# Kernel tuning notes

Measured on AMD Instinct MI355X. Metric: run time of the kernel, lower is better.

## Reference

```python
import jax, jax.numpy as jnp
import numpy as np

N_HEADS = 16

def _rotate_half(t):
    # t: [B, H, T, hs]; split last dim in half, return cat(-x2, x1)
    hs = t.shape[-1]
    x1, x2 = t[..., : hs // 2], t[..., hs // 2 :]
    return jnp.concatenate((-x2, x1), axis=-1)

def _rope_pos(T, hs, dtype):
    inv_freq = 1.0 / (10000.0 ** (jnp.arange(0, hs, 2, dtype=jnp.float32) / hs))
    freqs = jnp.arange(T, dtype=jnp.float32)[:, None] * inv_freq[None, :]  # [T, hs/2]
    pos = jnp.concatenate((freqs, freqs), axis=-1)  # [T, hs]
    return pos

def setup_inputs() -> dict:
    key = jax.random.key(0)
    ks = jax.random.split(key, 5)
    d = 2048
    x = jax.random.normal(ks[0], (2, 2048, d), dtype=jnp.float32)
    W_attn = jax.random.normal(ks[1], (d, 3 * d), dtype=jnp.float32) * (1.0 / np.sqrt(d))
    b_attn = jax.random.normal(ks[2], (3 * d,), dtype=jnp.float32) * 0.02
    W_proj = jax.random.normal(ks[3], (d, d), dtype=jnp.float32) * (1.0 / np.sqrt(d))
    b_proj = jax.random.normal(ks[4], (d,), dtype=jnp.float32) * 0.02
    return {"x": x, "W_attn": W_attn, "b_attn": b_attn, "W_proj": W_proj, "b_proj": b_proj}

def reference(x, W_attn, b_attn, W_proj, b_proj):
    B, T, C = x.shape
    nh = N_HEADS
    hs = C // nh
    qkv = x @ W_attn + b_attn  # [B, T, 3C]
    q, k, v = jnp.split(qkv, 3, axis=-1)
    # [B, T, C] -> [B, nh, T, hs]
    def to_heads(t):
        return t.reshape(B, T, nh, hs).transpose(0, 2, 1, 3)
    q, k, v = to_heads(q), to_heads(k), to_heads(v)
    # RoPE
    pos = _rope_pos(T, hs, x.dtype)  # [T, hs]
    cos, sin = jnp.cos(pos).astype(x.dtype), jnp.sin(pos).astype(x.dtype)
    q = q * cos + _rotate_half(q) * sin
    k = k * cos + _rotate_half(k) * sin
    # causal SDPA
    scale = 1.0 / np.sqrt(hs)
    scores = jnp.einsum('bhqd,bhkd->bhqk', q, k) * scale  # [B, nh, T, T]
    causal = jnp.tril(jnp.ones((T, T), dtype=bool))
    scores = jnp.where(causal, scores, jnp.finfo(scores.dtype).min)
    att = jax.nn.softmax(scores, axis=-1)
    out = jnp.einsum('bhqk,bhkd->bhqd', att, v)  # [B, nh, T, hs]
    y = out.transpose(0, 2, 1, 3).reshape(B, T, C)
    return y @ W_proj + b_proj
```

## Files before the change

kernel.cpp:

```cpp
#include <hip/hip_runtime.h>
#include <stdint.h>

typedef unsigned short u16;
typedef __attribute__((ext_vector_type(8))) short short8;
typedef __attribute__((ext_vector_type(4))) float f32x4;
typedef __attribute__((ext_vector_type(4))) unsigned short u16x4;

#define DEV __device__ __forceinline__

DEV u16 f2bf(float f) {
  union { float f; unsigned u; } v; v.f = f;
  unsigned r = v.u + 0x7fffu + ((v.u >> 16) & 1u);
  return (u16)(r >> 16);
}
DEV float bf2f(u16 b) {
  union { unsigned u; float f; } v; v.u = ((unsigned)b) << 16;
  return v.f;
}
DEV void gload_lds16(const void* g, void* l) {
  __builtin_amdgcn_global_load_lds((const __attribute__((address_space(1))) void*)g,
                                   (__attribute__((address_space(3))) void*)l,
                                   16, 0, 0);
}
DEV void block_barrier() {
  asm volatile("" ::: "memory");
  __builtin_amdgcn_s_barrier();
  asm volatile("" ::: "memory");
}

__global__ void k_conv(const float* __restrict__ in, u16* __restrict__ out, int n4) {
  int i = blockIdx.x * blockDim.x + threadIdx.x;
  if (i >= n4) return;
  const f32x4 v = *(const f32x4*)(in + (size_t)i * 4);
  u16x4 o;
  o[0] = f2bf(v[0]); o[1] = f2bf(v[1]); o[2] = f2bf(v[2]); o[3] = f2bf(v[3]);
  *(u16x4*)(out + (size_t)i * 4) = o;
}

__global__ void k_tconv(const float* __restrict__ in, u16* __restrict__ out, int R, int C) {
  __shared__ float tile[32][33];
  int c0 = blockIdx.x * 32, r0 = blockIdx.y * 32;
  int tx = threadIdx.x, ty = threadIdx.y;
#pragma unroll
  for (int j = 0; j < 32; j += 8)
    tile[ty + j][tx] = in[(size_t)(r0 + ty + j) * C + (c0 + tx)];
  __syncthreads();
#pragma unroll
  for (int j = 0; j < 32; j += 8)
    out[(size_t)(c0 + ty + j) * R + (r0 + tx)] = f2bf(tile[tx][ty + j]);
}

__global__ void k_rtab(float* __restrict__ ct, float* __restrict__ st) {
  int id = blockIdx.x * 256 + threadIdx.x;
  int t = id >> 6, dd = id & 63;
  float inv = exp2f((float)dd * -0.20762050593045077f);
  float s, c;
  sincosf((float)t * inv, &s, &c);
  ct[id] = c; st[id] = s;
}

__global__ __launch_bounds__(512, 2) void k_gemmqkv(const u16* __restrict__ A,
                                                    const u16* __restrict__ Bt,
                                                    const float* __restrict__ bias,
                                                    u16* __restrict__ qh,
                                                    u16* __restrict__ kh,
                                                    u16* __restrict__ vt,
                                                    const float* __restrict__ rtab) {
  const int Kld = 2048, nt = 32;
  __shared__ __align__(16) short smem[4][256 * 64];
  const int tid = threadIdx.x;
  const int wid = tid >> 6, lane = tid & 63;
  const int gx = gridDim.x;
  const int nwg = gx * gridDim.y;
  const int orig = blockIdx.y * gx + blockIdx.x;
  const int lg = (orig & 7) * (nwg >> 3) + (orig >> 3);
  const int bm = (lg % gx) * 256, bn = (lg / gx) * 256;
  const int wr = wid >> 2, wc = wid & 3;
  const int r = lane & 15, kq = lane >> 4, r7 = lane & 7;

  int aoff[4], boff[4], lbase[4];
#pragma unroll
  for (int j = 0; j < 4; ++j) {
    int c = j * 512 + wid * 64 + lane;
    int row = c >> 3, ch = c & 7;
    aoff[j] = (bm + row) * Kld + (ch ^ (row & 7)) * 8;
    boff[j] = (bn + row) * Kld + (ch ^ (row & 7)) * 8;
    lbase[j] = (j * 512 + wid * 64) * 16;
  }

#define STG_A(k0, buf, j) gload_lds16(A + aoff[j] + (k0), (char*)&smem[(buf)][0] + lbase[j])
#define STG_B(k0, buf, j) gload_lds16(Bt + boff[j] + (k0), (char*)&smem[2 + (buf)][0] + lbase[j])
#define RD_A(AF, MH, KK)                                                        \
  _Pragma("unroll")                                                             \
  for (int m2 = 0; m2 < 4; ++m2)                                                \
    AF[m2] = *(const short8*)&As[(wr * 128 + (MH) * 64 + m2 * 16 + r) * 64      \
                                 + (((KK) * 4 + kq) ^ r7) * 8];
#define RD_B(KK)                                                                \
  _Pragma("unroll")                                                             \
  for (int nf = 0; nf < 4; ++nf)                                                \
    bfr[KK][nf] = *(const short8*)&Bs[(wc * 64 + nf * 16 + r) * 64              \
                                      + (((KK) * 4 + kq) ^ r7) * 8];
#define PH_MFMA(AF, MH, KK)                                                     \
  __builtin_amdgcn_s_setprio(1);                                                \
  _Pragma("unroll")                                                             \
  for (int m2 = 0; m2 < 4; ++m2)                                                \
    _Pragma("unroll")                                                           \
    for (int nf = 0; nf < 4; ++nf)                                              \
      acc[(MH) * 4 + m2][nf] = __builtin_amdgcn_mfma_f32_16x16x32_bf16(         \
          AF[m2], bfr[KK][nf], acc[(MH) * 4 + m2][nf], 0, 0, 0);                \
  __builtin_amdgcn_s_setprio(0);

  f32x4 acc[8][4];
  const f32x4 zero = {0.f, 0.f, 0.f, 0.f};
#pragma unroll
  for (int i = 0; i < 8; ++i)
#pragma unroll
    for (int j = 0; j < 4; ++j) acc[i][j] = zero;

#pragma unroll
  for (int j = 0; j < 4; ++j) STG_A(0, 0, j);
#pragma unroll
  for (int j = 0; j < 4; ++j) STG_B(0, 0, j);
#pragma unroll
  for (int j = 0; j < 4; ++j) STG_B(64, 1, j);
  asm volatile("s_waitcnt vmcnt(4)" ::: "memory");
  block_barrier();

#pragma unroll 1
  for (int t = 0; t < nt; ++t) {
    const int cur = t & 1, nxt = cur ^ 1;
    const short* As = &smem[cur][0];
    const short* Bs = &smem[2 + cur][0];
    const int kA = (t + 1) * 64, kB = (t + 2) * 64;
    const bool sA = (t + 1 < nt), sB = (t + 2 < nt);
    short8 bfr[2][4];
    short8 af[4];

    RD_B(0)
    RD_A(af, 0, 0)
    if (sA) { STG_A(kA, nxt, 0); STG_A(kA, nxt, 1); }
    block_barrier();
    PH_MFMA(af, 0, 0)
    block_barrier();

    RD_B(1)
    RD_A(af, 0, 1)
    if (sA) { STG_A(kA, nxt, 2); STG_A(kA, nxt, 3); }
    block_barrier();
    PH_MFMA(af, 0, 1)
    block_barrier();

    RD_A(af, 1, 0)
    if (sB) { STG_B(kB, cur, 0); STG_B(kB, cur, 1); }
    block_barrier();
    PH_MFMA(af, 1, 0)
    block_barrier();

    RD_A(af, 1, 1)
    if (sB) { STG_B(kB, cur, 2); STG_B(kB, cur, 3); }
    block_barrier();
    PH_MFMA(af, 1, 1)
    if (t + 1 < nt) {
      if (sB) asm volatile("s_waitcnt vmcnt(4)" ::: "memory");
      else    asm volatile("s_waitcnt vmcnt(0)" ::: "memory");
    }
    block_barrier();
  }
#undef STG_A
#undef STG_B
#undef RD_A
#undef RD_B
#undef PH_MFMA

  const int by = lg / gx;
  const int part = by >> 3;
  const int b_ = bm >> 11;
  const int tb = bm & 2047;
  const int hbase = (bn & 2047) >> 7;
  u16* ob = (u16*)&smem[0][0];

#pragma unroll
  for (int nf = 0; nf < 4; ++nf) {
    int nl = wc * 64 + nf * 16 + r;
    float bv = bias[bn + nl];
#pragma unroll
    for (int mf = 0; mf < 8; ++mf) {
      int mlb = wr * 128 + mf * 16 + kq * 4;
#pragma unroll
      for (int i = 0; i < 4; ++i) {
        int ml = mlb + i;
        int cl = (part == 2)
          ? (nl ^ (((ml >> 2) & 3) << 4) ^ (((ml >> 4) & 7) << 1))
          : (nl ^ (((ml >> 2) & 3) << 4));
        ob[ml * 256 + cl] = f2bf(acc[mf][nf][i] + bv);
      }
    }
  }
  block_barrier();

  if (part == 2) {
#pragma unroll 1
    for (int iter = 0; iter < 32; ++iter) {
      int dl = iter * 8 + wid;
      int hh = hbase + (dl >> 7), d = dl & 127;
      int tl4 = lane * 4;
      int cl = dl ^ ((lane & 3) << 4) ^ (((lane >> 2) & 7) << 1);
      u16x4 o;
#pragma unroll
      for (int j = 0; j < 4; ++j) o[j] = ob[(tl4 + j) * 256 + cl];
      *(u16x4*)(vt + ((size_t)(b_ * 16 + hh) * 128 + d) * 2048 + tb + tl4) = o;
    }
  } else {
    u16* dst = part ? kh : qh;
    const float qscale = part ? 1.0f : 0.12751744766834352f;
    const int nl2 = lane * 4;
    const int hh = hbase + (nl2 >> 7);
    const int d0 = nl2 & 127;
    const int hi = (nl2 >> 6) & 1;
    const int dd4 = nl2 & 63;
    const float* ct = rtab;
    const float* st = rtab + 131072;
#pragma unroll 2
    for (int iter = 0; iter < 32; ++iter) {
      int tl = iter * 8 + wid;
      int tg = tb + tl;
      f32x4 c4 = *(const f32x4*)(ct + tg * 64 + dd4);
      f32x4 s4 = *(const f32x4*)(st + tg * 64 + dd4);
      int xr = ((tl >> 2) & 3) << 4;
      int base = tl * 256 + (nl2 ^ xr);
      int pbase = tl * 256 + ((nl2 ^ 64) ^ xr);
      u16x4 o;
#pragma unroll
      for (int j = 0; j < 4; ++j) {
        float vo = bf2f(ob[base + j]);
        float vp = bf2f(ob[pbase + j]);
        float vr = hi ? (vo * c4[j] + vp * s4[j]) : (vo * c4[j] - vp * s4[j]);
        o[j] = f2bf(vr * qscale);
      }
      *(u16x4*)(dst + ((size_t)(b_ * 16 + hh) * 2048 + tg) * 128 + d0) = o;
    }
  }
}

template <bool OUT_BF16, bool SPLITK>
__global__ __launch_bounds__(512, 2) void k_gemm3(const u16* __restrict__ A,
                                                  const u16* __restrict__ Bt,
                                                  const float* __restrict__ bias,
                                                  void* __restrict__ Cv,
                                                  int M, int N, int Kld, int nkt) {
  __shared__ __align__(16) short lA[2][256 * 64];
  __shared__ __align__(16) short lB[2][256 * 64];
  const int tid = threadIdx.x;
  const int wid = tid >> 6, lane = tid & 63;
  const int gx = gridDim.x;
  const int nwg = gx * gridDim.y;
  const int orig = blockIdx.y * gx + blockIdx.x;
  const int lg = (orig & 7) * (nwg >> 3) + (orig >> 3);
  const int bm = (lg % gx) * 256, bn = (lg / gx) * 256;
  const int wr = wid >> 2, wc = wid & 3;
  const int r = lane & 15, kq = lane >> 4, r7 = lane & 7;
  const int kz = SPLITK ? blockIdx.z * (nkt << 6) : 0;

  int aoff[4], boff[4], lbase[4];
#pragma unroll
  for (int j = 0; j < 4; ++j) {
    int c = j * 512 + wid * 64 + lane;
    int row = c >> 3, ch = c & 7;
    aoff[j] = (bm + row) * Kld + kz + (ch ^ (row & 7)) * 8;
    boff[j] = (bn + row) * Kld + kz + (ch ^ (row & 7)) * 8;
    lbase[j] = (j * 512 + wid * 64) * 16;
  }

#define STG_A(k0, buf, j) gload_lds16(A + aoff[j] + (k0), (char*)&lA[(buf)][0] + lbase[j])
#define STG_B(k0, buf, j) gload_lds16(Bt + boff[j] + (k0), (char*)&lB[(buf)][0] + lbase[j])
#define RD_A(AF, MH, KK)                                                        \
  _Pragma("unroll")                                                             \
  for (int m2 = 0; m2 < 4; ++m2)                                                \
    AF[m2] = *(const short8*)&As[(wr * 128 + (MH) * 64 + m2 * 16 + r) * 64      \
                                 + (((KK) * 4 + kq) ^ r7) * 8];
#define RD_B(KK)                                                                \
  _Pragma("unroll")                                                             \
  for (int nf = 0; nf < 4; ++nf)                                                \
    bfr[KK][nf] = *(const short8*)&Bs[(wc * 64 + nf * 16 + r) * 64              \
                                      + (((KK) * 4 + kq) ^ r7) * 8];
#define PH_MFMA(AF, MH, KK)                                                     \
  __builtin_amdgcn_s_setprio(1);                                                \
  _Pragma("unroll")                                                             \
  for (int m2 = 0; m2 < 4; ++m2)                                                \
    _Pragma("unroll")                                                           \
    for (int nf = 0; nf < 4; ++nf)                                              \
      acc[(MH) * 4 + m2][nf] = __builtin_amdgcn_mfma_f32_16x16x32_bf16(         \
          AF[m2], bfr[KK][nf], acc[(MH) * 4 + m2][nf], 0, 0, 0);                \
  __builtin_amdgcn_s_setprio(0);

  f32x4 acc[8][4];
  const f32x4 zero = {0.f, 0.f, 0.f, 0.f};
#pragma unroll
  for (int i = 0; i < 8; ++i)
#pragma unroll
    for (int j = 0; j < 4; ++j) acc[i][j] = zero;

  const int nt = nkt;

#pragma unroll
  for (int j = 0; j < 4; ++j) STG_A(0, 0, j);
#pragma unroll
  for (int j = 0; j < 4; ++j) STG_B(0, 0, j);
  if (nt > 1) {
#pragma unroll
    for (int j = 0; j < 4; ++j) STG_B(64, 1, j);
    asm volatile("s_waitcnt vmcnt(4)" ::: "memory");
  } else {
    asm volatile("s_waitcnt vmcnt(0)" ::: "memory");
  }
  block_barrier();

#pragma unroll 1
  for (int t = 0; t < nt; ++t) {
    const int cur = t & 1, nxt = cur ^ 1;
    const short* As = &lA[cur][0];
    const short* Bs = &lB[cur][0];
    const int kA = (t + 1) * 64, kB = (t + 2) * 64;
    const bool sA = (t + 1 < nt), sB = (t + 2 < nt);
    short8 bfr[2][4];
    short8 af[4];

    RD_B(0)
    RD_A(af, 0, 0)
    if (sA) { STG_A(kA, nxt, 0); STG_A(kA, nxt, 1); }
    block_barrier();
    PH_MFMA(af, 0, 0)
    block_barrier();

    RD_B(1)
    RD_A(af, 0, 1)
    if (sA) { STG_A(kA, nxt, 2); STG_A(kA, nxt, 3); }
    block_barrier();
    PH_MFMA(af, 0, 1)
    block_barrier();

    RD_A(af, 1, 0)
    if (sB) { STG_B(kB, cur, 0); STG_B(kB, cur, 1); }
    block_barrier();
    PH_MFMA(af, 1, 0)
    block_barrier();

    RD_A(af, 1, 1)
    if (sB) { STG_B(kB, cur, 2); STG_B(kB, cur, 3); }
    block_barrier();
    PH_MFMA(af, 1, 1)
    if (t + 1 < nt) {
      if (sB) asm volatile("s_waitcnt vmcnt(4)" ::: "memory");
      else    asm volatile("s_waitcnt vmcnt(0)" ::: "memory");
    }
    block_barrier();
  }
#undef STG_A
#undef STG_B
#undef RD_A
#undef RD_B
#undef PH_MFMA

#pragma unroll
  for (int mf = 0; mf < 8; ++mf)
#pragma unroll
    for (int nf = 0; nf < 4; ++nf) {
      int n = bn + wc * 64 + nf * 16 + r;
      float bv = SPLITK ? 0.f : bias[n];
#pragma unroll
      for (int i = 0; i < 4; ++i) {
        int m = bm + wr * 128 + mf * 16 + kq * 4 + i;
        float val = acc[mf][nf][i] + bv;
        if (SPLITK)
          ((float*)Cv)[(size_t)blockIdx.z * M * N + (size_t)m * N + n] = val;
        else if (OUT_BF16)
          ((u16*)Cv)[(size_t)m * N + n] = f2bf(val);
        else
          ((float*)Cv)[(size_t)m * N + n] = val;
      }
    }
}

__global__ void k_fadd(const float* __restrict__ p, const float* __restrict__ bias,
                       float* __restrict__ y, int n4) {
  const int half4 = 2097152;
  for (int i = blockIdx.x * blockDim.x + threadIdx.x; i < n4; i += gridDim.x * blockDim.x) {
    f32x4 a = *(const f32x4*)(p + (size_t)i * 4);
    f32x4 b = *(const f32x4*)(p + (size_t)(i + half4) * 4);
    f32x4 bv = *(const f32x4*)(bias + ((i & 511) << 2));
    f32x4 o = a + b + bv;
    *(f32x4*)(y + (size_t)i * 4) = o;
  }
}

__global__ __launch_bounds__(512) void k_attn(const u16* __restrict__ qh,
                                              const u16* __restrict__ kh,
                                              const u16* __restrict__ vt,
                                              u16* __restrict__ out) {
  __shared__ __align__(16) short lK[2][64 * 128];
  __shared__ __align__(16) short lV[2][128 * 64];
  __shared__ __align__(16) short lP[128 * 64];
  const int tid = threadIdx.x, wid = tid >> 6, lane = tid & 63;
  const int p = blockIdx.x, h = blockIdx.y, b = blockIdx.z;
  const size_t bh = (size_t)b * 16 + h;
  const u16* qb = qh + bh * 2048 * 128;
  const u16* kb = kh + bh * 2048 * 128;
  const u16* vb = vt + bh * 128 * 2048;
  const int r = lane & 15, kq = lane >> 4;
  const int r7 = r & 7;
  const int wrow = wid * 16;

  int koff[2], voff[2], lbase[2];
#pragma unroll
  for (int i = 0; i < 2; ++i) {
    int c = i * 512 + wid * 64 + lane;
    int krow = c >> 4, kch = c & 15;
    koff[i] = krow * 128 + ((kch ^ (krow & 7)) * 8);
    int vrow = c >> 3, vch = c & 7;
    voff[i] = vrow * 2048 + ((vch ^ (vrow & 7)) * 8);
    lbase[i] = (i * 512 + wid * 64) * 16;
  }

#pragma unroll 1
  for (int seg = 0; seg < 2; ++seg) {
    const int J = seg ? 15 - p : p;
    const int q0 = J * 128;
    const int nkt = 2 * J + 2;

    short8 qa[4];
#pragma unroll
    for (int kk = 0; kk < 4; ++kk)
      qa[kk] = *(const short8*)(qb + (size_t)(q0 + wrow + r) * 128 + kk * 32 + kq * 8);

    f32x4 O[8];
    const f32x4 zero = {0.f, 0.f, 0.f, 0.f};
#pragma unroll
    for (int nf = 0; nf < 8; ++nf) O[nf] = zero;
    float lp[4] = {0.f, 0.f, 0.f, 0.f};

#pragma unroll
    for (int i = 0; i < 2; ++i) {
      gload_lds16(kb + koff[i], (char*)&lK[0][0] + lbase[i]);
      gload_lds16(vb + voff[i], (char*)&lV[0][0] + lbase[i]);
    }

#pragma unroll 1
    for (int kt = 0; kt < nkt; ++kt) {
      const int cur = kt & 1;
      if (kt + 1 < nkt) {
        const size_t kbase = (size_t)(kt + 1) * 8192, vbase = (size_t)(kt + 1) * 64;
#pragma unroll
        for (int i = 0; i < 2; ++i) {
          gload_lds16(kb + kbase + koff[i], (char*)&lK[cur ^ 1][0] + lbase[i]);
          gload_lds16(vb + vbase + voff[i], (char*)&lV[cur ^ 1][0] + lbase[i]);
        }
        asm volatile("s_waitcnt vmcnt(4)" ::: "memory");
      } else {
        asm volatile("s_waitcnt vmcnt(0)" ::: "memory");
      }
      block_barrier();

      f32x4 S[4];
#pragma unroll
      for (int nf = 0; nf < 4; ++nf) S[nf] = zero;
#pragma unroll
      for (int kk = 0; kk < 4; ++kk) {
        short8 kf[4];
#pragma unroll
        for (int nf = 0; nf < 4; ++nf)
          kf[nf] = *(const short8*)&lK[cur][(nf * 16 + r) * 128 + ((kk * 4 + kq) ^ r7) * 8];
#pragma unroll
        for (int nf = 0; nf < 4; ++nf)
          S[nf] = __builtin_amdgcn_mfma_f32_16x16x32_bf16(qa[kk], kf[nf], S[nf], 0, 0, 0);
      }

      const bool diag = (kt >= nkt - 2);
#pragma unroll
      for (int nf = 0; nf < 4; ++nf)
#pragma unroll
        for (int i = 0; i < 4; ++i) {
          float pv = exp2f(S[nf][i]);
          if (diag) {
            int kg = kt * 64 + nf * 16 + r;
            int qg = q0 + wrow + kq * 4 + i;
            pv = (kg > qg) ? 0.f : pv;
          }
          lp[i] += pv;
          int row = wrow + kq * 4 + i;
          int cl = (nf * 2 + (r >> 3)) ^ ((kq * 4 + i) & 7);
          lP[row * 64 + cl * 8 + r7] = (short)f2bf(pv);
        }

#pragma unroll
      for (int kk = 0; kk < 2; ++kk) {
        short8 pa = *(const short8*)&lP[(wrow + r) * 64 + ((kk * 4 + kq) ^ r7) * 8];
#pragma unroll
        for (int nf = 0; nf < 8; ++nf) {
          short8 vf = *(const short8*)&lV[cur][(nf * 16 + r) * 64 + ((kk * 4 + kq) ^ r7) * 8];
          O[nf] = __builtin_amdgcn_mfma_f32_16x16x32_bf16(pa, vf, O[nf], 0, 0, 0);
        }
      }
      asm volatile("s_waitcnt lgkmcnt(0)" ::: "memory");
      block_barrier();
    }

    float inv[4];
#pragma unroll
    for (int i = 0; i < 4; ++i) {
      float v = lp[i];
      v += __shfl_xor(v, 1);
      v += __shfl_xor(v, 2);
      v += __shfl_xor(v, 4);
      v += __shfl_xor(v, 8);
      inv[i] = 1.f / v;
    }
#pragma unroll
    for (int nf = 0; nf < 8; ++nf)
#pragma unroll
      for (int i = 0; i < 4; ++i) {
        int qg = q0 + wrow + kq * 4 + i;
        out[(size_t)(b * 2048 + qg) * 2048 + h * 128 + nf * 16 + r] = f2bf(O[nf][i] * inv[i]);
      }
  }
}

extern "C" void kernel_launch(void* const* d_in, const int* in_sizes, int n_in,
                              void* d_out, int out_size, void* d_ws, size_t ws_size,
                              hipStream_t stream) {
  const float* x      = (const float*)d_in[0];
  const float* W_attn = (const float*)d_in[1];
  const float* b_attn = (const float*)d_in[2];
  const float* W_proj = (const float*)d_in[3];
  const float* b_proj = (const float*)d_in[4];
  float* y = (float*)d_out;

  u16* xb     = (u16*)d_ws;
  u16* wqkvT  = xb     + (size_t)4096 * 2048;
  u16* wprojT = wqkvT  + (size_t)6144 * 2048;
  u16* qkv    = wprojT + (size_t)2048 * 2048;
  u16* qh     = qkv    + (size_t)4096 * 6144;
  u16* kh     = qh     + (size_t)4096 * 2048;
  u16* vt     = kh     + (size_t)4096 * 2048;
  u16* attout = vt     + (size_t)4096 * 2048;
  if (ws_size < (size_t)83886080 * 2) return;

  float* rtab  = (float*)qkv;
  float* pproj = (float*)qkv;

  k_conv<<<8192, 256, 0, stream>>>(x, xb, 2097152);
  k_tconv<<<dim3(192, 64), dim3(32, 8), 0, stream>>>(W_attn, wqkvT, 2048, 6144);
  k_tconv<<<dim3(64, 64), dim3(32, 8), 0, stream>>>(W_proj, wprojT, 2048, 2048);
  k_rtab<<<512, 256, 0, stream>>>(rtab, rtab + 131072);
  k_gemmqkv<<<dim3(16, 24), 512, 0, stream>>>(xb, wqkvT, b_attn, qh, kh, vt, rtab);
  k_attn<<<dim3(8, 16, 2), 512, 0, stream>>>(qh, kh, vt, attout);
  k_gemm3<false, true><<<dim3(16, 8, 2), 512, 0, stream>>>(attout, wprojT, b_proj, pproj, 4096, 2048, 2048, 16);
  k_fadd<<<2048, 256, 0, stream>>>(pproj, b_proj, y, 2097152);
}
```

Measured before the change: 297.1 us.

## Merge prep kernels into one launch and restructure attention to 4-wave blocks

The conversion, weight transposes and RoPE table kernels become a single launch whose branch is chosen by block index, removing three launch gaps. The attention kernel drops from 8 to 4 waves per block, and each wave now computes two 16-row M fragments, so every K/V fragment read from LDS feeds twice as many MFMAs. It also launches one block per 128-row query tile (512 blocks) instead of pairing tiles J and 15-J inside one block, giving finer but less balanced work. The cost is more registers per wave and less cross-tile load balancing within a block.

New measurement: 300.5 us. Within noise of the previous version (+1.1%).

```diff
diff --git a/kernel.cpp b/kernel.cpp
--- a/kernel.cpp
+++ b/kernel.cpp
@@ -28,35 +28,42 @@
   asm volatile("" ::: "memory");
 }
 
-__global__ void k_conv(const float* __restrict__ in, u16* __restrict__ out, int n4) {
-  int i = blockIdx.x * blockDim.x + threadIdx.x;
-  if (i >= n4) return;
-  const f32x4 v = *(const f32x4*)(in + (size_t)i * 4);
-  u16x4 o;
-  o[0] = f2bf(v[0]); o[1] = f2bf(v[1]); o[2] = f2bf(v[2]); o[3] = f2bf(v[3]);
-  *(u16x4*)(out + (size_t)i * 4) = o;
-}
-
-__global__ void k_tconv(const float* __restrict__ in, u16* __restrict__ out, int R, int C) {
+__global__ void k_prep(const float* __restrict__ x, u16* __restrict__ xb,
+                       const float* __restrict__ Wa, u16* __restrict__ wqkvT,
+                       const float* __restrict__ Wp, u16* __restrict__ wprojT,
+                       float* __restrict__ ct, float* __restrict__ st) {
   __shared__ float tile[32][33];
-  int c0 = blockIdx.x * 32, r0 = blockIdx.y * 32;
-  int tx = threadIdx.x, ty = threadIdx.y;
-#pragma unroll
-  for (int j = 0; j < 32; j += 8)
-    tile[ty + j][tx] = in[(size_t)(r0 + ty + j) * C + (c0 + tx)];
-  __syncthreads();
-#pragma unroll
-  for (int j = 0; j < 32; j += 8)
-    out[(size_t)(c0 + ty + j) * R + (r0 + tx)] = f2bf(tile[tx][ty + j]);
-}
-
-__global__ void k_rtab(float* __restrict__ ct, float* __restrict__ st) {
-  int id = blockIdx.x * 256 + threadIdx.x;
-  int t = id >> 6, dd = id & 63;
-  float inv = exp2f((float)dd * -0.20762050593045077f);
-  float s, c;
-  sincosf((float)t * inv, &s, &c);
-  ct[id] = c; st[id] = s;
+  const int bid = blockIdx.x, tid = threadIdx.x;
+  if (bid < 8192) {
+    int i = bid * 256 + tid;
+    const f32x4 v = *(const f32x4*)(x + (size_t)i * 4);
+    u16x4 o;
+    o[0] = f2bf(v[0]); o[1] = f2bf(v[1]); o[2] = f2bf(v[2]); o[3] = f2bf(v[3]);
+    *(u16x4*)(xb + (size_t)i * 4) = o;
+  } else if (bid < 8192 + 12288 + 4096) {
+    const bool wa = bid < 8192 + 12288;
+    const int b2 = wa ? bid - 8192 : bid - 8192 - 12288;
+    const int gw = wa ? 192 : 64;
+    const float* in = wa ? Wa : Wp;
+    u16* out = wa ? wqkvT : wprojT;
+    const int C = wa ? 6144 : 2048;
+    const int c0 = (b2 % gw) * 32, r0 = (b2 / gw) * 32;
+    const int tx = tid & 31, ty = tid >> 5;
+#pragma unroll
+    for (int j = 0; j < 32; j += 8)
+      tile[ty + j][tx] = in[(size_t)(r0 + ty + j) * C + (c0 + tx)];
+    __syncthreads();
+#pragma unroll
+    for (int j = 0; j < 32; j += 8)
+      out[(size_t)(c0 + ty + j) * 2048 + (r0 + tx)] = f2bf(tile[tx][ty + j]);
+  } else {
+    int id = (bid - 24576) * 256 + tid;
+    int t = id >> 6, dd = id & 63;
+    float inv = exp2f((float)dd * -0.20762050593045077f);
+    float s, c;
+    sincosf((float)t * inv, &s, &c);
+    ct[id] = c; st[id] = s;
+  }
 }
 
 __global__ __launch_bounds__(512, 2) void k_gemmqkv(const u16* __restrict__ A,
@@ -393,7 +400,7 @@
   }
 }
 
-__global__ __launch_bounds__(512) void k_attn(const u16* __restrict__ qh,
+__global__ __launch_bounds__(256) void k_attn(const u16* __restrict__ qh,
                                               const u16* __restrict__ kh,
                                               const u16* __restrict__ vt,
                                               u16* __restrict__ out) {
@@ -401,113 +408,128 @@
   __shared__ __align__(16) short lV[2][128 * 64];
   __shared__ __align__(16) short lP[128 * 64];
   const int tid = threadIdx.x, wid = tid >> 6, lane = tid & 63;
-  const int p = blockIdx.x, h = blockIdx.y, b = blockIdx.z;
+  const int id = blockIdx.x;
+  const int jr = id & 15;
+  const int J = (id < 256) ? jr : 15 - jr;
+  const int h = (id >> 4) & 15, b = id >> 8;
+  const int q0 = J * 128;
+  const int nkt = 2 * J + 2;
   const size_t bh = (size_t)b * 16 + h;
   const u16* qb = qh + bh * 2048 * 128;
   const u16* kb = kh + bh * 2048 * 128;
   const u16* vb = vt + bh * 128 * 2048;
   const int r = lane & 15, kq = lane >> 4;
   const int r7 = r & 7;
-  const int wrow = wid * 16;
-
-  int koff[2], voff[2], lbase[2];
-#pragma unroll
-  for (int i = 0; i < 2; ++i) {
-    int c = i * 512 + wid * 64 + lane;
-    int krow = c >> 4, kch = c & 15;
+  const int wrow = wid * 32;
+
+  int koff[4], voff[4];
+#pragma unroll
+  for (int i = 0; i < 4; ++i) {
+    int ci = (wid * 4 + i) * 64 + lane;
+    int krow = ci >> 4, kch = ci & 15;
     koff[i] = krow * 128 + ((kch ^ (krow & 7)) * 8);
-    int vrow = c >> 3, vch = c & 7;
+    int vrow = ci >> 3, vch = ci & 7;
     voff[i] = vrow * 2048 + ((vch ^ (vrow & 7)) * 8);
-    lbase[i] = (i * 512 + wid * 64) * 16;
+  }
+
+  short8 qa[2][4];
+#pragma unroll
+  for (int mf = 0; mf < 2; ++mf)
+#pragma unroll
+    for (int kk = 0; kk < 4; ++kk)
+      qa[mf][kk] = *(const short8*)(qb + (size_t)(q0 + wrow + mf * 16 + r) * 128 + kk * 32 + kq * 8);
+
+  f32x4 O[2][8];
+  const f32x4 zero = {0.f, 0.f, 0.f, 0.f};
+#pragma unroll
+  for (int mf = 0; mf < 2; ++mf)
+#pragma unroll
+    for (int nf = 0; nf < 8; ++nf) O[mf][nf] = zero;
+  float lp[2][4] = {{0.f, 0.f, 0.f, 0.f}, {0.f, 0.f, 0.f, 0.f}};
+
+#pragma unroll
+  for (int i = 0; i < 4; ++i) {
+    gload_lds16(kb + koff[i], (char*)&lK[0][0] + (wid * 4 + i) * 1024);
+    gload_lds16(vb + voff[i], (char*)&lV[0][0] + (wid * 4 + i) * 1024);
   }
 
 #pragma unroll 1
-  for (int seg = 0; seg < 2; ++seg) {
-    const int J = seg ? 15 - p : p;
-    const int q0 = J * 128;
-    const int nkt = 2 * J + 2;
-
-    short8 qa[4];
-#pragma unroll
-    for (int kk = 0; kk < 4; ++kk)
-      qa[kk] = *(const short8*)(qb + (size_t)(q0 + wrow + r) * 128 + kk * 32 + kq * 8);
-
-    f32x4 O[8];
-    const f32x4 zero = {0.f, 0.f, 0.f, 0.f};
-#pragma unroll
-    for (int nf = 0; nf < 8; ++nf) O[nf] = zero;
-    float lp[4] = {0.f, 0.f, 0.f, 0.f};
-
-#pragma unroll
-    for (int i = 0; i < 2; ++i) {
-      gload_lds16(kb + koff[i], (char*)&lK[0][0] + lbase[i]);
-      gload_lds16(vb + voff[i], (char*)&lV[0][0] + lbase[i]);
-    }
-
-#pragma unroll 1
-    for (int kt = 0; kt < nkt; ++kt) {
-      const int cur = kt & 1;
-      if (kt + 1 < nkt) {
-        const size_t kbase = (size_t)(kt + 1) * 8192, vbase = (size_t)(kt + 1) * 64;
-#pragma unroll
-        for (int i = 0; i < 2; ++i) {
-          gload_lds16(kb + kbase + koff[i], (char*)&lK[cur ^ 1][0] + lbase[i]);
-          gload_lds16(vb + vbase + voff[i], (char*)&lV[cur ^ 1][0] + lbase[i]);
-        }
-        asm volatile("s_waitcnt vmcnt(4)" ::: "memory");
-      } else {
-        asm volatile("s_waitcnt vmcnt(0)" ::: "memory");
+  for (int kt = 0; kt < nkt; ++kt) {
+    const int cur = kt & 1;
+    if (kt + 1 < nkt) {
+      const size_t kbase = (size_t)(kt + 1) * 8192, vbase = (size_t)(kt + 1) * 64;
+#pragma unroll
+      for (int i = 0; i < 4; ++i) {
+        gload_lds16(kb + kbase + koff[i], (char*)&lK[cur ^ 1][0] + (wid * 4 + i) * 1024);
+        gload_lds16(vb + vbase + voff[i], (char*)&lV[cur ^ 1][0] + (wid * 4 + i) * 1024);
       }
-      block_barrier();
-
-      f32x4 S[4];
-#pragma unroll
-      for (int nf = 0; nf < 4; ++nf) S[nf] = zero;
-#pragma unroll
-      for (int kk = 0; kk < 4; ++kk) {
-        short8 kf[4];
+      asm volatile("s_waitcnt vmcnt(8)" ::: "memory");
+    } else {
+      asm volatile("s_waitcnt vmcnt(0)" ::: "memory");
+    }
+    block_barrier();
+
+    f32x4 S[2][4];
+#pragma unroll
+    for (int mf = 0; mf < 2; ++mf)
+#pragma unroll
+      for (int nf = 0; nf < 4; ++nf) S[mf][nf] = zero;
+#pragma unroll
+    for (int kk = 0; kk < 4; ++kk) {
+      short8 kf[4];
+#pragma unroll
+      for (int nf = 0; nf < 4; ++nf)
+        kf[nf] = *(const short8*)&lK[cur][(nf * 16 + r) * 128 + ((kk * 4 + kq) ^ r7) * 8];
+#pragma unroll
+      for (int mf = 0; mf < 2; ++mf)
 #pragma unroll
         for (int nf = 0; nf < 4; ++nf)
-          kf[nf] = *(const short8*)&lK[cur][(nf * 16 + r) * 128 + ((kk * 4 + kq) ^ r7) * 8];
-#pragma unroll
-        for (int nf = 0; nf < 4; ++nf)
-          S[nf] = __builtin_amdgcn_mfma_f32_16x16x32_bf16(qa[kk], kf[nf], S[nf], 0, 0, 0);
-      }
-
-      const bool diag = (kt >= nkt - 2);
+          S[mf][nf] = __builtin_amdgcn_mfma_f32_16x16x32_bf16(qa[mf][kk], kf[nf], S[mf][nf], 0, 0, 0);
+    }
+
+    const bool diag = (kt >= nkt - 2);
+#pragma unroll
+    for (int mf = 0; mf < 2; ++mf)
 #pragma unroll
       for (int nf = 0; nf < 4; ++nf)
 #pragma unroll
         for (int i = 0; i < 4; ++i) {
-          float pv = exp2f(S[nf][i]);
+          float pv = exp2f(S[mf][nf][i]);
           if (diag) {
             int kg = kt * 64 + nf * 16 + r;
-            int qg = q0 + wrow + kq * 4 + i;
+            int qg = q0 + wrow + mf * 16 + kq * 4 + i;
             pv = (kg > qg) ? 0.f : pv;
           }
-          lp[i] += pv;
-          int row = wrow + kq * 4 + i;
+          lp[mf][i] += pv;
+          int row = wrow + mf * 16 + kq * 4 + i;
           int cl = (nf * 2 + (r >> 3)) ^ ((kq * 4 + i) & 7);
           lP[row * 64 + cl * 8 + r7] = (short)f2bf(pv);
         }
 
 #pragma unroll
-      for (int kk = 0; kk < 2; ++kk) {
-        short8 pa = *(const short8*)&lP[(wrow + r) * 64 + ((kk * 4 + kq) ^ r7) * 8];
-#pragma unroll
-        for (int nf = 0; nf < 8; ++nf) {
-          short8 vf = *(const short8*)&lV[cur][(nf * 16 + r) * 64 + ((kk * 4 + kq) ^ r7) * 8];
-          O[nf] = __builtin_amdgcn_mfma_f32_16x16x32_bf16(pa, vf, O[nf], 0, 0, 0);
-        }
+    for (int kk = 0; kk < 2; ++kk) {
+      short8 pa[2];
+#pragma unroll
+      for (int mf = 0; mf < 2; ++mf)
+        pa[mf] = *(const short8*)&lP[(wrow + mf * 16 + r) * 64 + ((kk * 4 + kq) ^ r7) * 8];
+#pragma unroll
+      for (int nf = 0; nf < 8; ++nf) {
+        short8 vf = *(const short8*)&lV[cur][(nf * 16 + r) * 64 + ((kk * 4 + kq) ^ r7) * 8];
+#pragma unroll
+        for (int mf = 0; mf < 2; ++mf)
+          O[mf][nf] = __builtin_amdgcn_mfma_f32_16x16x32_bf16(pa[mf], vf, O[mf][nf], 0, 0, 0);
       }
-      asm volatile("s_waitcnt lgkmcnt(0)" ::: "memory");
-      block_barrier();
-    }
-
+    }
+    asm volatile("s_waitcnt lgkmcnt(0)" ::: "memory");
+    block_barrier();
+  }
+
+#pragma unroll
+  for (int mf = 0; mf < 2; ++mf) {
     float inv[4];
 #pragma unroll
     for (int i = 0; i < 4; ++i) {
-      float v = lp[i];
+      float v = lp[mf][i];
       v += __shfl_xor(v, 1);
       v += __shfl_xor(v, 2);
       v += __shfl_xor(v, 4);
@@ -518,8 +540,8 @@
     for (int nf = 0; nf < 8; ++nf)
 #pragma unroll
       for (int i = 0; i < 4; ++i) {
-        int qg = q0 + wrow + kq * 4 + i;
-        out[(size_t)(b * 2048 + qg) * 2048 + h * 128 + nf * 16 + r] = f2bf(O[nf][i] * inv[i]);
+        int qg = q0 + wrow + mf * 16 + kq * 4 + i;
+        out[(size_t)(b * 2048 + qg) * 2048 + h * 128 + nf * 16 + r] = f2bf(O[mf][nf][i] * inv[i]);
       }
   }
 }
@@ -547,12 +569,9 @@
   float* rtab  = (float*)qkv;
   float* pproj = (float*)qkv;
 
-  k_conv<<<8192, 256, 0, stream>>>(x, xb, 2097152);
-  k_tconv<<<dim3(192, 64), dim3(32, 8), 0, stream>>>(W_attn, wqkvT, 2048, 6144);
-  k_tconv<<<dim3(64, 64), dim3(32, 8), 0, stream>>>(W_proj, wprojT, 2048, 2048);
-  k_rtab<<<512, 256, 0, stream>>>(rtab, rtab + 131072);
+  k_prep<<<25088, 256, 0, stream>>>(x, xb, W_attn, wqkvT, W_proj, wprojT, rtab, rtab + 131072);
   k_gemmqkv<<<dim3(16, 24), 512, 0, stream>>>(xb, wqkvT, b_attn, qh, kh, vt, rtab);
-  k_attn<<<dim3(8, 16, 2), 512, 0, stream>>>(qh, kh, vt, attout);
+  k_attn<<<512, 256, 0, stream>>>(qh, kh, vt, attout);
   k_gemm3<false, true><<<dim3(16, 8, 2), 512, 0, stream>>>(attout, wprojT, b_proj, pproj, 4096, 2048, 2048, 16);
   k_fadd<<<2048, 256, 0, stream>>>(pproj, b_proj, y, 2097152);
 }
```
